# Optimization experiments

Hardware: AMD Instinct MI355X
Metric: run time of the kernel (lower is better)

The kernel has to match this reference:

```python
import jax, jax.numpy as jnp
import numpy as np

B, N, DIN, DOUT = 8, 2048, 512, 256
NUM_BUCKETS = 20


def setup_inputs() -> dict:
    key = jax.random.key(0)
    ks = jax.random.split(key, 12)
    s_in = 1.0 / np.sqrt(DIN)
    s_out = 1.0 / np.sqrt(DOUT)
    return {
        "x": jax.random.normal(ks[0], (B, N, DIN), dtype=jnp.float32),
        "price_rank": jax.random.randint(ks[1], (B, N), 0, N, dtype=jnp.int64),
        "Wq": jax.random.uniform(ks[2], (DOUT, DIN), jnp.float32, -s_in, s_in),
        "bq": jax.random.uniform(ks[3], (DOUT,), jnp.float32, -s_in, s_in),
        "Wk": jax.random.uniform(ks[4], (DOUT, DIN), jnp.float32, -s_in, s_in),
        "bk": jax.random.uniform(ks[5], (DOUT,), jnp.float32, -s_in, s_in),
        "Wv": jax.random.uniform(ks[6], (DOUT, DIN), jnp.float32, -s_in, s_in),
        "bv": jax.random.uniform(ks[7], (DOUT,), jnp.float32, -s_in, s_in),
        "Ws": jax.random.uniform(ks[8], (1, DOUT), jnp.float32, -s_out, s_out),
        "bs": jax.random.uniform(ks[9], (1,), jnp.float32, -s_out, s_out),
        "rank_emb": jax.random.normal(ks[10], (NUM_BUCKETS, 1), dtype=jnp.float32),
        "rank_w": jnp.ones((1,), dtype=jnp.float32),
    }


def reference(x, price_rank, Wq, bq, Wk, bk, Wv, bv, Ws, bs, rank_emb, rank_w):
    scale = jnp.sqrt(jnp.asarray(DOUT, dtype=x.dtype))
    q = jnp.einsum("bnd,od->bno", x, Wq) + bq  # [B,N,DOUT]
    k = jnp.einsum("bnd,od->bno", x, Wk) + bk
    v = jnp.einsum("bnd,od->bno", x, Wv) + bv
    scores = jnp.einsum("bno,bmo->bnm", q, k) / scale  # [B,N,N]
    # learned pairwise rank-distance bias gate
    rank_dist = jnp.abs(price_rank[:, :, None] - price_rank[:, None, :])
    buckets = jnp.clip(rank_dist // 5, 0, NUM_BUCKETS - 1)  # [B,N,N] int
    prior = rank_emb[buckets, 0]  # gather embedding, squeeze last dim
    gate = jax.nn.sigmoid(rank_w[0] * prior)
    scores = scores * gate
    attn = jax.nn.softmax(scores, axis=2)
    context = jnp.einsum("bnm,bmo->bno", attn, v)  # [B,N,DOUT]
    winner = jax.nn.sigmoid(jnp.einsum("bno,uo->bnu", context, Ws) + bs)[..., 0]
    return winner  # [B,N]
```

## Files before the change

kernel.cpp:

```cpp
#include <hip/hip_runtime.h>
#include <hip/hip_bf16.h>

#define B_    8
#define N_    2048
#define DIN_  512
#define DOUT_ 256
#define NBUCK 20

typedef __attribute__((ext_vector_type(8))) short  short8;
typedef __attribute__((ext_vector_type(4))) float  floatx4;

__device__ __forceinline__ unsigned short f2b(float f) {
    __hip_bfloat16 h = __float2bfloat16(f);
    unsigned short u;
    __builtin_memcpy(&u, &h, 2);
    return u;
}

__device__ __forceinline__ void load_lds16(const unsigned short* g, unsigned short* l) {
    __builtin_amdgcn_global_load_lds(
        (const __attribute__((address_space(1))) unsigned int*)g,
        (__attribute__((address_space(3))) unsigned int*)l, 16, 0, 0);
}

__global__ __launch_bounds__(256) void prep_kernel(
    const float* __restrict__ wq, const float* __restrict__ wk,
    const float* __restrict__ Wv, const float* __restrict__ Ws,
    const float* __restrict__ bv,
    unsigned short* __restrict__ dst, float* __restrict__ wvs,
    float* __restrict__ bvs) {
    const int blk = blockIdx.x, tid = threadIdx.x;
    if (blk < 128) {
        int i = (blk * 256 + tid) * 8;
        const float* src = (i < 131072) ? (wq + i) : (wk + (i - 131072));
        float4 a = *(const float4*)(src);
        float4 b = *(const float4*)(src + 4);
        uint4 r;
        r.x = f2b(a.x) | ((unsigned)f2b(a.y) << 16);
        r.y = f2b(a.z) | ((unsigned)f2b(a.w) << 16);
        r.z = f2b(b.x) | ((unsigned)f2b(b.y) << 16);
        r.w = f2b(b.z) | ((unsigned)f2b(b.w) << 16);
        *(uint4*)(dst + i) = r;
    } else {
        __shared__ float wsl[DOUT_];
        wsl[tid] = Ws[tid];
        __syncthreads();
        if (tid < 128) {
            int d = (blk - 128) * 128 + tid;
            float s = 0.f;
#pragma unroll 8
            for (int o = 0; o < DOUT_; ++o) s += Wv[(size_t)o * DIN_ + d] * wsl[o];
            wvs[d] = s;
        }
        if (blk == 128 && tid < 64) {
            float bb = wsl[tid] * bv[tid] + wsl[tid + 64] * bv[tid + 64] +
                       wsl[tid + 128] * bv[tid + 128] + wsl[tid + 192] * bv[tid + 192];
            for (int off = 1; off < 64; off <<= 1) bb += __shfl_xor(bb, off, 64);
            if (tid == 0) *bvs = bb;
        }
    }
}

__global__ __launch_bounds__(256) void cvt_x_kernel(const float* __restrict__ x,
                                                    const float* __restrict__ wvs,
                                                    const float* __restrict__ bvs,
                                                    unsigned short* __restrict__ xb,
                                                    float* __restrict__ vw) {
    int tid = threadIdx.x, wave = tid >> 6, lane = tid & 63;
    int row = blockIdx.x * 4 + wave;
    size_t base = (size_t)row * DIN_ + lane * 8;
    float4 a = *(const float4*)(x + base);
    float4 b = *(const float4*)(x + base + 4);
    float4 wa = *(const float4*)(wvs + lane * 8);
    float4 wb = *(const float4*)(wvs + lane * 8 + 4);
    uint4 r;
    r.x = f2b(a.x) | ((unsigned)f2b(a.y) << 16);
    r.y = f2b(a.z) | ((unsigned)f2b(a.w) << 16);
    r.z = f2b(b.x) | ((unsigned)f2b(b.y) << 16);
    r.w = f2b(b.z) | ((unsigned)f2b(b.w) << 16);
    *(uint4*)(xb + base) = r;
    float d = a.x * wa.x + a.y * wa.y + a.z * wa.z + a.w * wa.w +
              b.x * wb.x + b.y * wb.y + b.z * wb.z + b.w * wb.w;
    for (int off = 1; off < 64; off <<= 1) d += __shfl_xor(d, off, 64);
    if (lane == 0) vw[row] = d + *bvs;
}

__global__ __launch_bounds__(256, 2) void qkv_kernel(
    const unsigned short* __restrict__ xb, const unsigned short* __restrict__ wb,
    const float* __restrict__ bq, const float* __restrict__ bk,
    unsigned short* __restrict__ qo, unsigned short* __restrict__ ko) {
    __shared__ unsigned short alds[128 * 32];
    __shared__ unsigned short blds[128 * 32];
    const int g = blockIdx.x;
    const int xcd = g & 7, t2 = g >> 3;
    const int colBlk = t2 & 3, rowGrp = t2 >> 2;
    const int rowBlk = rowGrp * 8 + xcd;
    const int tid = threadIdx.x;
    const int wave = tid >> 6, lane = tid & 63, quad = lane >> 4, l16 = lane & 15;
    const int wr = wave >> 1, wc = wave & 1;
    const int row0 = rowBlk * 128, col0 = colBlk * 128;

    floatx4 acc[4][4];
#pragma unroll
    for (int i = 0; i < 4; ++i)
#pragma unroll
        for (int j = 0; j < 4; ++j) acc[i][j] = (floatx4){0.f, 0.f, 0.f, 0.f};

    const unsigned short* ag = xb + (size_t)(row0 + (tid >> 2)) * DIN_ + (tid & 3) * 8;
    const unsigned short* bg = wb + (size_t)(col0 + (tid >> 2)) * DIN_ + (tid & 3) * 8;
    unsigned short* alw0 = alds + (size_t)(wave * 64) * 8;
    unsigned short* alw1 = alds + (size_t)(256 + wave * 64) * 8;
    unsigned short* blw0 = blds + (size_t)(wave * 64) * 8;
    unsigned short* blw1 = blds + (size_t)(256 + wave * 64) * 8;

#pragma unroll 1
    for (int kc = 0; kc < DIN_; kc += 32) {
        __syncthreads();
        load_lds16(ag + kc, alw0);
        load_lds16(ag + (size_t)64 * DIN_ + kc, alw1);
        load_lds16(bg + kc, blw0);
        load_lds16(bg + (size_t)64 * DIN_ + kc, blw1);
        __syncthreads();
        short8 af[4], bf[4];
#pragma unroll
        for (int f = 0; f < 4; ++f) {
            af[f] = *(const short8*)&alds[(size_t)(wr * 64 + f * 16 + l16) * 32 + quad * 8];
            bf[f] = *(const short8*)&blds[(size_t)(wc * 64 + f * 16 + l16) * 32 + quad * 8];
        }
#pragma unroll
        for (int i = 0; i < 4; ++i)
#pragma unroll
            for (int j = 0; j < 4; ++j)
                acc[i][j] = __builtin_amdgcn_mfma_f32_16x16x32_bf16(af[i], bf[j], acc[i][j], 0, 0, 0);
    }

#pragma unroll
    for (int j = 0; j < 4; ++j) {
        int col = col0 + wc * 64 + j * 16 + l16;
        unsigned short* dst = (col < 256) ? qo : ko;
        float bias = (col < 256) ? bq[col] : bk[col - 256];
        int c = col & 255;
#pragma unroll
        for (int i = 0; i < 4; ++i)
#pragma unroll
            for (int r = 0; r < 4; ++r) {
                int row = row0 + wr * 64 + i * 16 + quad * 4 + r;
                dst[(size_t)row * DOUT_ + c] = f2b(acc[i][j][r] + bias);
            }
    }
}

__global__ __launch_bounds__(512, 2) void attn_kernel(
    const unsigned short* __restrict__ q, const unsigned short* __restrict__ k,
    const float* __restrict__ vw, const int* __restrict__ pr,
    const float* __restrict__ rank_emb, const float* __restrict__ rank_w,
    const float* __restrict__ bs, float* __restrict__ out) {
    const int g = blockIdx.x;
    const int b = g & 7, rblk = g >> 3;
    const int tid = threadIdx.x, wave = tid >> 6, lane = tid & 63;
    const int quad = lane >> 4, l16 = lane & 15;
    const int n0 = rblk * 64;
    const int sw = l16 & 7;

    __shared__ unsigned short klds[2][8][4096];
    __shared__ float gtab[NBUCK];
    __shared__ float lL[8][64], wdL[8][64];

    if (tid < NBUCK)
        gtab[tid] = 0.0625f * 1.44269504f / (1.f + __expf(-rank_w[0] * rank_emb[tid]));
    __syncthreads();

    const unsigned short* qb = q + (size_t)b * N_ * DOUT_;
    const unsigned short* kb = k + (size_t)b * N_ * DOUT_;
    const float* vwb = vw + b * N_;
    const int* prb = pr + b * N_;

    short8 qf[4][8];
#pragma unroll
    for (int a = 0; a < 4; ++a)
#pragma unroll
        for (int c = 0; c < 8; ++c)
            qf[a][c] = *(const short8*)(qb + (size_t)(n0 + a * 16 + l16) * DOUT_ + c * 32 + quad * 8);

    float prn5[4][4];
#pragma unroll
    for (int a = 0; a < 4; ++a)
#pragma unroll
        for (int r = 0; r < 4; ++r)
            prn5[a][r] = (float)prb[n0 + a * 16 + quad * 4 + r] * 0.2f;

    float lacc[4][4], wacc[4][4];
#pragma unroll
    for (int a = 0; a < 4; ++a)
#pragma unroll
        for (int r = 0; r < 4; ++r) { lacc[a][r] = 0.f; wacc[a][r] = 0.f; }

    const int srow = lane >> 5;
    const int spos = lane & 31;
    const unsigned short* kwb = kb + (size_t)(wave * 16) * DOUT_;
    unsigned short* buf0 = &klds[0][wave][0];
    unsigned short* buf1 = &klds[1][wave][0];
    const int colbase = wave * 16 + l16;

    int   prm_raw = prb[colbase];
    float vwv_cur = vwb[colbase];

#pragma unroll
    for (int i = 0; i < 8; ++i) {
        int row = i * 2 + srow;
        int gseg = spos ^ (row & 7);
        load_lds16(kwb + (size_t)row * DOUT_ + gseg * 8, buf0 + i * 512);
    }

#pragma unroll 1
    for (int j = 0; j < 16; ++j) {
        unsigned short* bufc = (j & 1) ? buf1 : buf0;
        unsigned short* bufn = (j & 1) ? buf0 : buf1;

        floatx4 s[4];
#pragma unroll
        for (int a = 0; a < 4; ++a) s[a] = (floatx4){0.f, 0.f, 0.f, 0.f};
#pragma unroll
        for (int c = 0; c < 8; ++c) {
            int seg = (quad + 4 * c) ^ sw;
            short8 kf = *(const short8*)&bufc[((size_t)l16 * 32 + seg) * 8];
            s[0] = __builtin_amdgcn_mfma_f32_16x16x32_bf16(qf[0][c], kf, s[0], 0, 0, 0);
            s[1] = __builtin_amdgcn_mfma_f32_16x16x32_bf16(qf[1][c], kf, s[1], 0, 0, 0);
            s[2] = __builtin_amdgcn_mfma_f32_16x16x32_bf16(qf[2][c], kf, s[2], 0, 0, 0);
            s[3] = __builtin_amdgcn_mfma_f32_16x16x32_bf16(qf[3][c], kf, s[3], 0, 0, 0);
        }
        int nxtcol = ((j < 15) ? (j + 1) * 128 : j * 128) + colbase;
        int   prm_nxt = prb[nxtcol];
        float vwv_nxt = vwb[nxtcol];
        if (j < 15) {
            const unsigned short* src = kwb + (size_t)(j + 1) * 128 * DOUT_;
#pragma unroll
            for (int i = 0; i < 8; ++i) {
                int row = i * 2 + srow;
                int gseg = spos ^ (row & 7);
                load_lds16(src + (size_t)row * DOUT_ + gseg * 8, bufn + i * 512);
            }
        }
        float prm5 = (float)prm_raw * 0.2f;
#pragma unroll
        for (int a = 0; a < 4; ++a)
#pragma unroll
            for (int r = 0; r < 4; ++r) {
                float d5 = fabsf(prn5[a][r] - prm5);
                int idx = (int)fminf(d5, 19.0f);
                float p = exp2f(s[a][r] * gtab[idx]);
                lacc[a][r] += p;
                wacc[a][r] += p * vwv_cur;
            }
        prm_raw = prm_nxt;
        vwv_cur = vwv_nxt;
    }

#pragma unroll
    for (int off = 1; off < 16; off <<= 1) {
#pragma unroll
        for (int a = 0; a < 4; ++a)
#pragma unroll
            for (int r = 0; r < 4; ++r) {
                lacc[a][r] += __shfl_xor(lacc[a][r], off, 64);
                wacc[a][r] += __shfl_xor(wacc[a][r], off, 64);
            }
    }
    if (l16 == 0) {
#pragma unroll
        for (int a = 0; a < 4; ++a)
#pragma unroll
            for (int r = 0; r < 4; ++r) {
                int row = a * 16 + quad * 4 + r;
                lL[wave][row]  = lacc[a][r];
                wdL[wave][row] = wacc[a][r];
            }
    }
    __syncthreads();
    if (tid < 64) {
        float l = 0.f, wd = 0.f;
#pragma unroll
        for (int s2 = 0; s2 < 8; ++s2) { l += lL[s2][tid]; wd += wdL[s2][tid]; }
        float logit = wd / l + bs[0];
        out[(size_t)b * N_ + n0 + tid] = 1.f / (1.f + __expf(-logit));
    }
}

extern "C" void kernel_launch(void* const* d_in, const int* in_sizes, int n_in,
                              void* d_out, int out_size, void* d_ws, size_t ws_size,
                              hipStream_t stream) {
    const float* x   = (const float*)d_in[0];
    const int*   pr  = (const int*)d_in[1];
    const float* Wq  = (const float*)d_in[2];
    const float* bq  = (const float*)d_in[3];
    const float* Wk  = (const float*)d_in[4];
    const float* bk  = (const float*)d_in[5];
    const float* Wv  = (const float*)d_in[6];
    const float* bv  = (const float*)d_in[7];
    const float* Ws  = (const float*)d_in[8];
    const float* bs  = (const float*)d_in[9];
    const float* remb = (const float*)d_in[10];
    const float* rw   = (const float*)d_in[11];
    float* out = (float*)d_out;

    char* ws = (char*)d_ws;
    unsigned short* xb  = (unsigned short*)ws;
    unsigned short* wb  = (unsigned short*)(ws + 16777216);
    unsigned short* q   = (unsigned short*)(ws + 17301504);
    unsigned short* kk  = (unsigned short*)(ws + 25690112);
    float*          vwp = (float*)(ws + 34078720);
    float*          wvs = (float*)(ws + 34144256);
    float*          bvs = (float*)(ws + 34146304);

    hipLaunchKernelGGL(prep_kernel, dim3(132), dim3(256), 0, stream,
                       Wq, Wk, Wv, Ws, bv, wb, wvs, bvs);
    hipLaunchKernelGGL(cvt_x_kernel, dim3(4096), dim3(256), 0, stream, x, wvs, bvs, xb, vwp);
    hipLaunchKernelGGL(qkv_kernel, dim3(512), dim3(256), 0, stream,
                       xb, wb, bq, bk, q, kk);
    hipLaunchKernelGGL(attn_kernel, dim3(256), dim3(512), 0, stream,
                       q, kk, vwp, pr, remb, rw, bs, out);
}
```

Baseline: 160.6 us.

## Double-buffer QKV GEMM LDS tiles with larger K step, swizzle, and MFMA priority

The QK projection GEMM now uses double-buffered LDS tiles with a K step of 64 instead of 32. The next tile's global-to-LDS loads are issued before the current tile's MFMAs, so one barrier per iteration replaces two. An XOR swizzle on LDS segments is added to reduce bank conflicts. The attention kernel also wraps its QK MFMA loop in s_setprio to favor matrix issue. LDS use per block grows fourfold (64KB), which may reduce occupancy against the launch bounds of 2 blocks.

```diff
diff --git a/kernel.cpp b/kernel.cpp
--- a/kernel.cpp
+++ b/kernel.cpp
@@ -89,8 +89,8 @@
     const unsigned short* __restrict__ xb, const unsigned short* __restrict__ wb,
     const float* __restrict__ bq, const float* __restrict__ bk,
     unsigned short* __restrict__ qo, unsigned short* __restrict__ ko) {
-    __shared__ unsigned short alds[128 * 32];
-    __shared__ unsigned short blds[128 * 32];
+    __shared__ unsigned short alds[2][128 * 64];
+    __shared__ unsigned short blds[2][128 * 64];
     const int g = blockIdx.x;
     const int xcd = g & 7, t2 = g >> 3;
     const int colBlk = t2 & 3, rowGrp = t2 >> 2;
@@ -99,6 +99,7 @@
     const int wave = tid >> 6, lane = tid & 63, quad = lane >> 4, l16 = lane & 15;
     const int wr = wave >> 1, wc = wave & 1;
     const int row0 = rowBlk * 128, col0 = colBlk * 128;
+    const int sw3 = l16 & 7;
 
     floatx4 acc[4][4];
 #pragma unroll
@@ -106,32 +107,49 @@
 #pragma unroll
         for (int j = 0; j < 4; ++j) acc[i][j] = (floatx4){0.f, 0.f, 0.f, 0.f};
 
-    const unsigned short* ag = xb + (size_t)(row0 + (tid >> 2)) * DIN_ + (tid & 3) * 8;
-    const unsigned short* bg = wb + (size_t)(col0 + (tid >> 2)) * DIN_ + (tid & 3) * 8;
-    unsigned short* alw0 = alds + (size_t)(wave * 64) * 8;
-    unsigned short* alw1 = alds + (size_t)(256 + wave * 64) * 8;
-    unsigned short* blw0 = blds + (size_t)(wave * 64) * 8;
-    unsigned short* blw1 = blds + (size_t)(256 + wave * 64) * 8;
+    const int gseg = (lane & 7) ^ (lane >> 3);
+    const unsigned short* ag = xb + (size_t)(row0 + wave * 8 + (lane >> 3)) * DIN_ + gseg * 8;
+    const unsigned short* bg = wb + (size_t)(col0 + wave * 8 + (lane >> 3)) * DIN_ + gseg * 8;
+
+#pragma unroll
+    for (int i = 0; i < 4; ++i) {
+        load_lds16(ag + (size_t)i * 32 * DIN_, &alds[0][wave * 512 + i * 2048]);
+        load_lds16(bg + (size_t)i * 32 * DIN_, &blds[0][wave * 512 + i * 2048]);
+    }
+    __syncthreads();
 
 #pragma unroll 1
-    for (int kc = 0; kc < DIN_; kc += 32) {
+    for (int t = 0; t < 8; ++t) {
+        const unsigned short* al = (t & 1) ? alds[1] : alds[0];
+        const unsigned short* bl = (t & 1) ? blds[1] : blds[0];
+        unsigned short* aln = (t & 1) ? &alds[0][0] : &alds[1][0];
+        unsigned short* bln = (t & 1) ? &blds[0][0] : &blds[1][0];
+        if (t < 7) {
+            size_t koff = (size_t)(t + 1) * 64;
+#pragma unroll
+            for (int i = 0; i < 4; ++i) {
+                load_lds16(ag + (size_t)i * 32 * DIN_ + koff, aln + wave * 512 + i * 2048);
+                load_lds16(bg + (size_t)i * 32 * DIN_ + koff, bln + wave * 512 + i * 2048);
+            }
+        }
+#pragma unroll
+        for (int h = 0; h < 2; ++h) {
+            short8 af[4], bf[4];
+#pragma unroll
+            for (int f = 0; f < 4; ++f) {
+                int ar = wr * 64 + f * 16 + l16;
+                int br = wc * 64 + f * 16 + l16;
+                int s  = (h * 4 + quad) ^ sw3;
+                af[f] = *(const short8*)&al[(size_t)ar * 64 + s * 8];
+                bf[f] = *(const short8*)&bl[(size_t)br * 64 + s * 8];
+            }
+#pragma unroll
+            for (int i = 0; i < 4; ++i)
+#pragma unroll
+                for (int j = 0; j < 4; ++j)
+                    acc[i][j] = __builtin_amdgcn_mfma_f32_16x16x32_bf16(af[i], bf[j], acc[i][j], 0, 0, 0);
+        }
         __syncthreads();
-        load_lds16(ag + kc, alw0);
-        load_lds16(ag + (size_t)64 * DIN_ + kc, alw1);
-        load_lds16(bg + kc, blw0);
-        load_lds16(bg + (size_t)64 * DIN_ + kc, blw1);
-        __syncthreads();
-        short8 af[4], bf[4];
-#pragma unroll
-        for (int f = 0; f < 4; ++f) {
-            af[f] = *(const short8*)&alds[(size_t)(wr * 64 + f * 16 + l16) * 32 + quad * 8];
-            bf[f] = *(const short8*)&blds[(size_t)(wc * 64 + f * 16 + l16) * 32 + quad * 8];
-        }
-#pragma unroll
-        for (int i = 0; i < 4; ++i)
-#pragma unroll
-            for (int j = 0; j < 4; ++j)
-                acc[i][j] = __builtin_amdgcn_mfma_f32_16x16x32_bf16(af[i], bf[j], acc[i][j], 0, 0, 0);
     }
 
 #pragma unroll
@@ -220,6 +238,7 @@
         floatx4 s[4];
 #pragma unroll
         for (int a = 0; a < 4; ++a) s[a] = (floatx4){0.f, 0.f, 0.f, 0.f};
+        __builtin_amdgcn_s_setprio(1);
 #pragma unroll
         for (int c = 0; c < 8; ++c) {
             int seg = (quad + 4 * c) ^ sw;
@@ -229,6 +248,7 @@
             s[2] = __builtin_amdgcn_mfma_f32_16x16x32_bf16(qf[2][c], kf, s[2], 0, 0, 0);
             s[3] = __builtin_amdgcn_mfma_f32_16x16x32_bf16(qf[3][c], kf, s[3], 0, 0, 0);
         }
+        __builtin_amdgcn_s_setprio(0);
         int nxtcol = ((j < 15) ? (j + 1) * 128 : j * 128) + colbase;
         int   prm_nxt = prb[nxtcol];
         float vwv_nxt = vwb[nxtcol];
```

Result: faster. 156.4 us (-2.6%).
